# Performance work log

Measured on AMD Instinct MI355X. Metric: run time of the kernel, lower is better.

## Reference

```python
import jax, jax.numpy as jnp
import numpy as np

B, S, D, H, L, DFF, NI, AD = 8, 512, 512, 8, 4, 2048, 20000, 128
DK = D // H


def _make_pe(max_len, d):
    pos = np.arange(max_len, dtype=np.float32)[:, None]
    div = np.exp(np.arange(0, d, 2, dtype=np.float32) * (-np.log(10000.0) / d))
    pe = np.zeros((max_len, d), dtype=np.float32)
    pe[:, 0::2] = np.sin(pos * div)
    pe[:, 1::2] = np.cos(pos * div)
    return jnp.asarray(pe)


def setup_inputs() -> dict:
    key = jax.random.key(0)
    ks = iter(jax.random.split(key, 64))
    def nrm(shape):
        return jax.random.normal(next(ks), shape, jnp.float32) * 0.02
    inp = {
        'item_ids': jax.random.randint(next(ks), (B, S), 0, NI),
        'audio_features': jax.random.normal(next(ks), (B, S, AD), jnp.float32),
        'is_organic': jax.random.bernoulli(next(ks), 0.5, (B, S)).astype(jnp.float32),
        'padding_mask': jnp.ones((B, 1, 1, S), jnp.float32),
        'emb_table': nrm((NI + 1, D)),
        'pe': _make_pe(S, D),
        'Wa1': nrm((AD, D)), 'ba1': jnp.zeros((D,)),
        'Wa2': nrm((D, D)), 'ba2': jnp.zeros((D,)),
        'Wf': nrm((2 * D, D)), 'bf': jnp.zeros((D,)),
        'Wq': nrm((L, D, D)), 'bq': jnp.zeros((L, D)),
        'Wk': nrm((L, D, D)), 'bk': jnp.zeros((L, D)),
        'Wv': nrm((L, D, D)), 'bv': jnp.zeros((L, D)),
        'Wo': nrm((L, D, D)), 'bo': jnp.zeros((L, D)),
        'worg': nrm((L, H)), 'borg': jnp.zeros((L, H)),
        'ln1s': jnp.ones((L, D)), 'ln1b': jnp.zeros((L, D)),
        'ln2s': jnp.ones((L, D)), 'ln2b': jnp.zeros((L, D)),
        'Wff1': nrm((L, D, DFF)), 'bff1': jnp.zeros((L, DFF)),
        'Wff2': nrm((L, DFF, D)), 'bff2': jnp.zeros((L, D)),
        'lnOs': jnp.ones((D,)), 'lnOb': jnp.zeros((D,)),
        'Wg': nrm((D + 1, D)), 'bg': jnp.zeros((D,)),
        'Wout': nrm((D, NI)), 'bout': jnp.zeros((NI,)),
    }
    return inp


def _ln(x, s, b, eps=1e-5):
    m = jnp.mean(x, -1, keepdims=True)
    v = jnp.mean((x - m) ** 2, -1, keepdims=True)
    return (x - m) * jax.lax.rsqrt(v + eps) * s + b


def reference(item_ids, audio_features, is_organic, padding_mask, emb_table, pe,
              Wa1, ba1, Wa2, ba2, Wf, bf, Wq, bq, Wk, bk, Wv, bv, Wo, bo,
              worg, borg, ln1s, ln1b, ln2s, ln2b, Wff1, bff1, Wff2, bff2,
              lnOs, lnOb, Wg, bg, Wout, bout):
    b_, s_ = item_ids.shape
    scale = 1.0 / np.sqrt(DK).astype(np.float32)
    tbl = emb_table.at[0].set(0.0)  # padding_idx=0
    item_emb = tbl[item_ids]                                    # (B,S,D)
    audio_emb = jax.nn.relu(audio_features @ Wa1 + ba1) @ Wa2 + ba2
    x = jax.nn.relu(jnp.concatenate([item_emb, audio_emb], -1) @ Wf + bf)
    x = x + pe[:s_]
    for l in range(L):
        q = (x @ Wq[l] + bq[l]).reshape(b_, s_, H, DK).transpose(0, 2, 1, 3)
        k = (x @ Wk[l] + bk[l]).reshape(b_, s_, H, DK).transpose(0, 2, 1, 3)
        v = (x @ Wv[l] + bv[l]).reshape(b_, s_, H, DK).transpose(0, 2, 1, 3)
        scores = jnp.einsum('bhqd,bhkd->bhqk', q, k) * scale    # (B,H,S,S)
        org = is_organic[:, :, None] * worg[l] + borg[l]        # (B,S,H)
        scores = scores + org.transpose(0, 2, 1)[..., None]     # per-query bias
        scores = jnp.where(padding_mask == 0, -1e9, scores)
        attn = jax.nn.softmax(scores, -1)
        ctx = jnp.einsum('bhqk,bhkd->bhqd', attn, v)
        ctx = ctx.transpose(0, 2, 1, 3).reshape(b_, s_, D)
        x = _ln(x + ctx @ Wo[l] + bo[l], ln1s[l], ln1b[l])
        ff = jax.nn.relu(x @ Wff1[l] + bff1[l]) @ Wff2[l] + bff2[l]
        x = _ln(x + ff, ln2s[l], ln2b[l])
    x = _ln(x, lnOs, lnOb)
    gate = jax.nn.sigmoid(jnp.concatenate([x, is_organic[..., None]], -1) @ Wg + bg)
    logits = (x * gate) @ Wout + bout                           # (B,S,NI)
    return logits
```

## Files before the change

### kernel.cpp

```cpp
#include <hip/hip_runtime.h>
#include <hip/hip_bf16.h>

typedef float f32x4 __attribute__((ext_vector_type(4)));
typedef __bf16 bf16x8 __attribute__((ext_vector_type(8)));

#define DEV __device__ __forceinline__

constexpr int B_ = 8, S_ = 512, D_ = 512, H_ = 8, L_ = 4, DFF_ = 2048, NI_ = 20000, AD_ = 128, DK_ = 64;
constexpr int N_ = B_ * S_;
constexpr int NOUT_PAD = 20096;

DEV void gload_lds16(const void* g, void* l) {
  __builtin_amdgcn_global_load_lds((const __attribute__((address_space(1))) unsigned int*)g,
                                   (__attribute__((address_space(3))) unsigned int*)l, 16, 0, 0);
}

DEV int xcd_swizzle(int bid, int nwg) {
  int q = nwg >> 3, r = nwg & 7;
  int x = bid & 7, idx = bid >> 3;
  int base = (x < r) ? x * (q + 1) : r * (q + 1) + (x - r) * q;
  return base + idx;
}

template<int BM, int BN, int EPI, int ACT, int NT>
__global__ __launch_bounds__(256)
void gemm2(const __hip_bfloat16* __restrict__ A, int lda,
           const __hip_bfloat16* __restrict__ Bm, int ldb,
           void* __restrict__ Cv, int ldc,
           const float* __restrict__ bias,
           const void* __restrict__ p1, const void* __restrict__ p2,
           const void* __restrict__ p3,
           int K, int Ncols)
{
  constexpr int BK = 64;
  constexpr int MI = BM / 32, NJ = BN / 32;
  constexpr int LA = BM * BK / 2048, LB = BN * BK / 2048;
  __shared__ __align__(16) unsigned short smA[2][BM * BK];
  __shared__ __align__(16) unsigned short smB[2][BN * BK];

  const int nwg = gridDim.x * gridDim.y;
  const int bid = blockIdx.y * gridDim.x + blockIdx.x;
  const int wgid = xcd_swizzle(bid, nwg);
  const int m0 = (wgid % gridDim.x) * BM, n0 = (wgid / gridDim.x) * BN;

  const int tid = threadIdx.x, wv = tid >> 6, lane = tid & 63;
  const int l15 = lane & 15, l4 = lane >> 4;
  const int wm = (wv >> 1) * (BM / 2), wn = (wv & 1) * (BN / 2);

  auto stage = [&](int buf, int k0) {
#pragma unroll
    for (int it = 0; it < LA; ++it) {
      int idx = it * 256 + tid, row = idx >> 3, c = idx & 7;
      int sc = c ^ (row & 7);
      gload_lds16((const void*)(A + (size_t)(m0 + row) * lda + k0 + sc * 8),
                  (void*)&smA[buf][(size_t)(it * 256 + wv * 64) * 8]);
    }
#pragma unroll
    for (int it = 0; it < LB; ++it) {
      int idx = it * 256 + tid, row = idx >> 3, c = idx & 7;
      int sc = c ^ (row & 7);
      gload_lds16((const void*)(Bm + (size_t)(n0 + row) * ldb + k0 + sc * 8),
                  (void*)&smB[buf][(size_t)(it * 256 + wv * 64) * 8]);
    }
  };

  f32x4 acc[MI][NJ];
#pragma unroll
  for (int i = 0; i < MI; ++i)
#pragma unroll
    for (int j = 0; j < NJ; ++j) acc[i][j] = f32x4{0.f, 0.f, 0.f, 0.f};

  const int nk = K / BK;
  stage(0, 0);
  __syncthreads();

  int cur = 0;
  for (int t = 0; t < nk; ++t) {
    if (t + 1 < nk) stage(cur ^ 1, (t + 1) * BK);

    bf16x8 af[MI][2], bfr[NJ][2];
#pragma unroll
    for (int i = 0; i < MI; ++i)
#pragma unroll
      for (int kk = 0; kk < 2; ++kk) {
        int row = wm + i * 16 + l15;
        int ch = (kk * 4 + l4) ^ (row & 7);
        af[i][kk] = *reinterpret_cast<const bf16x8*>(&smA[cur][row * BK + ch * 8]);
      }
#pragma unroll
    for (int j = 0; j < NJ; ++j)
#pragma unroll
      for (int kk = 0; kk < 2; ++kk) {
        int row = wn + j * 16 + l15;
        int ch = (kk * 4 + l4) ^ (row & 7);
        bfr[j][kk] = *reinterpret_cast<const bf16x8*>(&smB[cur][row * BK + ch * 8]);
      }
    __builtin_amdgcn_s_setprio(1);
#pragma unroll
    for (int kk = 0; kk < 2; ++kk)
#pragma unroll
      for (int i = 0; i < MI; ++i)
#pragma unroll
        for (int j = 0; j < NJ; ++j)
          acc[i][j] = __builtin_amdgcn_mfma_f32_16x16x32_bf16(af[i][kk], bfr[j][kk], acc[i][j], 0, 0, 0);
    __builtin_amdgcn_s_setprio(0);
    __syncthreads();
    cur ^= 1;
  }

#pragma unroll
  for (int i = 0; i < MI; ++i) {
#pragma unroll
    for (int j = 0; j < NJ; ++j) {
#pragma unroll
      for (int r = 0; r < 4; ++r) {
        int row = m0 + wm + i * 16 + l4 * 4 + r;
        int col = n0 + wn + j * 16 + l15;
        if (col < Ncols) {
          float v = acc[i][j][r];
          if (bias) v += bias[col];
          if (ACT == 1) v = v > 0.f ? v : 0.f;
          if constexpr (EPI == 0) {
            float* dst = &((float*)Cv)[(size_t)row * ldc + col];
            if constexpr (NT) __builtin_nontemporal_store(v, dst);
            else *dst = v;
          } else if constexpr (EPI == 1) {
            ((__hip_bfloat16*)Cv)[(size_t)row * ldc + col] = __float2bfloat16(v);
          } else if constexpr (EPI == 2) {
            v += ((const float*)p2)[(size_t)(row & 511) * 512 + col];
            ((float*)Cv)[(size_t)row * ldc + col] = v;
            ((__hip_bfloat16*)p1)[(size_t)row * ldc + col] = __float2bfloat16(v);
          } else if constexpr (EPI == 3) {
            if (col < 1024) {
              ((__hip_bfloat16*)Cv)[(size_t)(col >> 9) * N_ * 512 + (size_t)row * 512 + (col & 511)] =
                  __float2bfloat16(v);
            } else {
              int hd = col - 1024, b = row >> 9, s = row & 511;
              ((__hip_bfloat16*)p1)[((size_t)(b * 8 + (hd >> 6)) * 64 + (hd & 63)) * 512 + s] =
                  __float2bfloat16(v);
            }
          } else if constexpr (EPI == 4) {
            float zz = v + ((const float*)p2)[row] * ((const float*)p3)[col];
            float sg = 1.f / (1.f + __expf(-zz));
            float xn = ((const float*)p1)[(size_t)row * 512 + col];
            ((__hip_bfloat16*)Cv)[(size_t)row * 512 + col] = __float2bfloat16(xn * sg);
          }
        }
      }
    }
  }
}

__global__ __launch_bounds__(256)
void k_flash(const __hip_bfloat16* __restrict__ q, const __hip_bfloat16* __restrict__ k,
             const __hip_bfloat16* __restrict__ vt, const float* __restrict__ mask,
             __hip_bfloat16* __restrict__ ctx)
{
  __shared__ __align__(16) unsigned short Ql[64 * 64];
  __shared__ __align__(16) unsigned short Kl[2][64 * 64];
  __shared__ __align__(16) unsigned short Vl[2][64 * 64];
  __shared__ __align__(16) unsigned short Pl[4][16 * 64];

  const int qt = blockIdx.x, bh = blockIdx.y;
  const int b = bh >> 3, h = bh & 7;
  const int tid = threadIdx.x, wv = tid >> 6, lane = tid & 63;
  const int l15 = lane & 15, l4 = lane >> 4;
  const int q0 = qt * 64;

  const __hip_bfloat16* Qg = q + ((size_t)(b * 512 + q0) * 512) + h * 64;
  const __hip_bfloat16* Kg = k + ((size_t)(b * 512) * 512) + h * 64;
  const __hip_bfloat16* Vg = vt + ((size_t)bh * 64) * 512;
  const float* mk = mask + b * 512;

  auto stageQ = [&]() {
#pragma unroll
    for (int it = 0; it < 2; ++it) {
      int idx = it * 256 + wv * 64 + lane;
      int row = idx >> 3, c = idx & 7;
      gload_lds16((const void*)(Qg + (size_t)row * 512 + (c ^ (row & 7)) * 8),
                  (void*)&Ql[(it * 256 + wv * 64) * 8]);
    }
  };
  auto stageKV = [&](int buf, int kv0) {
#pragma unroll
    for (int it = 0; it < 2; ++it) {
      int idx = it * 256 + wv * 64 + lane;
      int row = idx >> 3, c = idx & 7;
      gload_lds16((const void*)(Kg + (size_t)(kv0 + row) * 512 + (c ^ (row & 7)) * 8),
                  (void*)&Kl[buf][(it * 256 + wv * 64) * 8]);
    }
#pragma unroll
    for (int it = 0; it < 2; ++it) {
      int idx = it * 256 + wv * 64 + lane;
      int row = idx >> 3, c = idx & 7;
      gload_lds16((const void*)(Vg + (size_t)row * 512 + kv0 + (c ^ (row & 7)) * 8),
                  (void*)&Vl[buf][(it * 256 + wv * 64) * 8]);
    }
  };

  stageQ();
  stageKV(0, 0);
  __syncthreads();

  bf16x8 aq[2];
#pragma unroll
  for (int kk = 0; kk < 2; ++kk) {
    int row = wv * 16 + l15;
    aq[kk] = *reinterpret_cast<const bf16x8*>(
        &Ql[row * 64 + (((kk * 4 + l4) ^ (row & 7)) * 8)]);
  }

  f32x4 accO[4];
  float mrun[4], lrun[4];
#pragma unroll
  for (int j = 0; j < 4; ++j) accO[j] = f32x4{0.f, 0.f, 0.f, 0.f};
#pragma unroll
  for (int r = 0; r < 4; ++r) { mrun[r] = -3e38f; lrun[r] = 0.f; }

  int cur = 0;
  for (int t = 0; t < 8; ++t) {
    if (t + 1 < 8) stageKV(cur ^ 1, (t + 1) * 64);
    const int kv0 = t * 64;

    f32x4 s[4];
#pragma unroll
    for (int j = 0; j < 4; ++j) s[j] = f32x4{0.f, 0.f, 0.f, 0.f};
#pragma unroll
    for (int kk = 0; kk < 2; ++kk) {
#pragma unroll
      for (int j = 0; j < 4; ++j) {
        int row = j * 16 + l15;
        bf16x8 bk = *reinterpret_cast<const bf16x8*>(
            &Kl[cur][row * 64 + (((kk * 4 + l4) ^ (row & 7)) * 8)]);
        s[j] = __builtin_amdgcn_mfma_f32_16x16x32_bf16(aq[kk], bk, s[j], 0, 0, 0);
      }
    }

#pragma unroll
    for (int j = 0; j < 4; ++j) {
      float mval = mk[kv0 + j * 16 + l15];
#pragma unroll
      for (int r = 0; r < 4; ++r)
        s[j][r] = (mval == 0.f) ? -1e30f : s[j][r];
    }

    float alpha[4];
#pragma unroll
    for (int r = 0; r < 4; ++r) {
      float v = fmaxf(fmaxf(s[0][r], s[1][r]), fmaxf(s[2][r], s[3][r]));
      v = fmaxf(v, __shfl_xor(v, 1));
      v = fmaxf(v, __shfl_xor(v, 2));
      v = fmaxf(v, __shfl_xor(v, 4));
      v = fmaxf(v, __shfl_xor(v, 8));
      float mn = fmaxf(mrun[r], v);
      alpha[r] = __expf(mrun[r] - mn);
      mrun[r] = mn;
    }
    float rs[4] = {0.f, 0.f, 0.f, 0.f};
#pragma unroll
    for (int j = 0; j < 4; ++j)
#pragma unroll
      for (int r = 0; r < 4; ++r) {
        float p = __expf(s[j][r] - mrun[r]);
        s[j][r] = p;
        rs[r] += p;
      }
#pragma unroll
    for (int r = 0; r < 4; ++r) {
      float v = rs[r];
      v += __shfl_xor(v, 1); v += __shfl_xor(v, 2);
      v += __shfl_xor(v, 4); v += __shfl_xor(v, 8);
      lrun[r] = lrun[r] * alpha[r] + v;
#pragma unroll
      for (int j = 0; j < 4; ++j) accO[j][r] *= alpha[r];
    }

#pragma unroll
    for (int j = 0; j < 4; ++j)
#pragma unroll
      for (int r = 0; r < 4; ++r) {
        int qrow = l4 * 4 + r, key = j * 16 + l15;
        __hip_bfloat16 hb = __float2bfloat16(s[j][r]);
        Pl[wv][qrow * 64 + (((key >> 3) ^ (qrow & 7)) * 8) + (key & 7)] =
            *reinterpret_cast<unsigned short*>(&hb);
      }

#pragma unroll
    for (int kc = 0; kc < 2; ++kc) {
      bf16x8 ap = *reinterpret_cast<const bf16x8*>(
          &Pl[wv][l15 * 64 + (((kc * 4 + l4) ^ (l15 & 7)) * 8)]);
#pragma unroll
      for (int j = 0; j < 4; ++j) {
        int row = j * 16 + l15;
        bf16x8 bv2 = *reinterpret_cast<const bf16x8*>(
            &Vl[cur][row * 64 + (((kc * 4 + l4) ^ (row & 7)) * 8)]);
        accO[j] = __builtin_amdgcn_mfma_f32_16x16x32_bf16(ap, bv2, accO[j], 0, 0, 0);
      }
    }
    __syncthreads();
    cur ^= 1;
  }

#pragma unroll
  for (int r = 0; r < 4; ++r) {
    float inv = lrun[r] > 0.f ? 1.f / lrun[r] : 0.f;
#pragma unroll
    for (int j = 0; j < 4; ++j) {
      int row = q0 + wv * 16 + l4 * 4 + r;
      int col = h * 64 + j * 16 + l15;
      ctx[(size_t)(b * 512 + row) * 512 + col] = __float2bfloat16(accO[j][r] * inv);
    }
  }
}

__global__ void k_transpose(const float* __restrict__ in, __hip_bfloat16* __restrict__ out,
                            int K, int N, long inBatch, long outBatch, float scale)
{
  __shared__ float tile[32][33];
  int z = blockIdx.z;
  const float* ip = in + (long)z * inBatch;
  __hip_bfloat16* op = out + (long)z * outBatch;
  int n0 = blockIdx.x * 32, k0 = blockIdx.y * 32;
  int tx = threadIdx.x, ty = threadIdx.y;
#pragma unroll
  for (int r = 0; r < 4; ++r) {
    int k = k0 + ty + r * 8, n = n0 + tx;
    if (k < K && n < N) tile[ty + r * 8][tx] = ip[(size_t)k * N + n];
  }
  __syncthreads();
#pragma unroll
  for (int r = 0; r < 4; ++r) {
    int n = n0 + ty + r * 8, k = k0 + tx;
    if (n < N && k < K) op[(size_t)n * K + k] = __float2bfloat16(tile[tx][ty + r * 8] * scale);
  }
}

__global__ void k_cvt(const float* __restrict__ in, __hip_bfloat16* __restrict__ out) {
  int i = blockIdx.x * 256 + threadIdx.x;
  out[i] = __float2bfloat16(in[i]);
}

__global__ void k_packbias(const float* __restrict__ bq, const float* __restrict__ bk,
                           const float* __restrict__ bv, float* __restrict__ out) {
  int i = blockIdx.x * 256 + threadIdx.x;
  int d = i & 511, t = (i >> 9) % 3, l = i / (3 * 512);
  const float* src = (t == 0) ? bq : (t == 1) ? bk : bv;
  out[i] = src[l * 512 + d] * (t == 0 ? 0.125f : 1.f);
}

__global__ void k_gather(const int* __restrict__ ids, const float* __restrict__ tbl,
                         __hip_bfloat16* __restrict__ cat) {
  int n = blockIdx.x, t = threadIdx.x;
  int id = ids[n];
  const float* src = tbl + (size_t)id * 512;
  size_t dst = (size_t)n * 1024;
  float a0 = (id == 0) ? 0.f : src[t];
  float a1 = (id == 0) ? 0.f : src[t + 256];
  cat[dst + t] = __float2bfloat16(a0);
  cat[dst + t + 256] = __float2bfloat16(a1);
}

__global__ void k_ln(const float* __restrict__ x, const float* __restrict__ y,
                     const float* __restrict__ gam, const float* __restrict__ bet,
                     float* __restrict__ xout, __hip_bfloat16* __restrict__ xb) {
  int row = blockIdx.x, t = threadIdx.x;
  size_t base = (size_t)row * 512;
  float v0 = x[base + t], v1 = x[base + t + 256];
  if (y) { v0 += y[base + t]; v1 += y[base + t + 256]; }
  __shared__ float sm[4];
  float s = v0 + v1;
  for (int o = 32; o; o >>= 1) s += __shfl_xor(s, o);
  if ((t & 63) == 0) sm[t >> 6] = s;
  __syncthreads();
  float mean = (sm[0] + sm[1] + sm[2] + sm[3]) * (1.f / 512.f);
  __syncthreads();
  float d0 = v0 - mean, d1 = v1 - mean;
  float qq = d0 * d0 + d1 * d1;
  for (int o = 32; o; o >>= 1) qq += __shfl_xor(qq, o);
  if ((t & 63) == 0) sm[t >> 6] = qq;
  __syncthreads();
  float var = (sm[0] + sm[1] + sm[2] + sm[3]) * (1.f / 512.f);
  float rs = rsqrtf(var + 1e-5f);
  float o0 = d0 * rs * gam[t] + bet[t];
  float o1 = d1 * rs * gam[t + 256] + bet[t + 256];
  xout[base + t] = o0;
  xout[base + t + 256] = o1;
  xb[base + t] = __float2bfloat16(o0);
  xb[base + t + 256] = __float2bfloat16(o1);
}

extern "C" void kernel_launch(void* const* d_in, const int* in_sizes, int n_in,
                              void* d_out, int out_size, void* d_ws, size_t ws_size,
                              hipStream_t stream) {
  typedef __hip_bfloat16 bf;
  const int*   item_ids = (const int*)  d_in[0];
  const float* audio    = (const float*)d_in[1];
  const float* organic  = (const float*)d_in[2];
  const float* mask     = (const float*)d_in[3];
  const float* emb      = (const float*)d_in[4];
  const float* pe       = (const float*)d_in[5];
  const float* Wa1 = (const float*)d_in[6],  *ba1 = (const float*)d_in[7];
  const float* Wa2 = (const float*)d_in[8],  *ba2 = (const float*)d_in[9];
  const float* Wf  = (const float*)d_in[10], *bfb = (const float*)d_in[11];
  const float* Wq  = (const float*)d_in[12], *bq  = (const float*)d_in[13];
  const float* Wk  = (const float*)d_in[14], *bk  = (const float*)d_in[15];
  const float* Wv  = (const float*)d_in[16], *bv  = (const float*)d_in[17];
  const float* Wo  = (const float*)d_in[18], *bo  = (const float*)d_in[19];
  const float* ln1s = (const float*)d_in[22], *ln1b = (const float*)d_in[23];
  const float* ln2s = (const float*)d_in[24], *ln2b = (const float*)d_in[25];
  const float* Wff1 = (const float*)d_in[26], *bff1 = (const float*)d_in[27];
  const float* Wff2 = (const float*)d_in[28], *bff2 = (const float*)d_in[29];
  const float* lnOs = (const float*)d_in[30], *lnOb = (const float*)d_in[31];
  const float* Wg   = (const float*)d_in[32], *bg   = (const float*)d_in[33];
  const float* Wout = (const float*)d_in[34], *bout = (const float*)d_in[35];
  float* out = (float*)d_out;

  char* ws = (char*)d_ws;
  size_t off = 0;
  auto alloc = [&](size_t bytes) -> char* {
    char* p = ws + off;
    off = (off + bytes + 255) & ~(size_t)255;
    return p;
  };
  bf* Wa1T = (bf*)alloc((size_t)512 * 128 * 2);
  bf* Wa2T = (bf*)alloc((size_t)512 * 512 * 2);
  bf* WfT  = (bf*)alloc((size_t)512 * 1024 * 2);
  bf* WqkvT = (bf*)alloc((size_t)L_ * 3 * D_ * D_ * 2);
  bf* WoT  = (bf*)alloc((size_t)L_ * D_ * D_ * 2);
  bf* Wff1T = (bf*)alloc((size_t)L_ * DFF_ * D_ * 2);
  bf* Wff2T = (bf*)alloc((size_t)L_ * D_ * DFF_ * 2);
  bf* WgT   = (bf*)alloc((size_t)512 * 512 * 2);
  bf* WoutT = (bf*)alloc((size_t)NOUT_PAD * 512 * 2);
  float* bqkv = (float*)alloc((size_t)L_ * 3 * 512 * 4);
  bf* ab    = (bf*)alloc((size_t)N_ * AD_ * 2);
  bf* cat   = (bf*)alloc((size_t)N_ * 1024 * 2);
  bf* ah    = (bf*)alloc((size_t)N_ * 512 * 2);
  float* xf = (float*)alloc((size_t)N_ * 512 * 4);
  bf* xb    = (bf*)alloc((size_t)N_ * 512 * 2);
  bf* qkv   = (bf*)alloc((size_t)3 * N_ * 512 * 2);
  bf* vt    = (bf*)alloc((size_t)B_ * H_ * DK_ * S_ * 2);
  bf* ctxb  = (bf*)alloc((size_t)N_ * 512 * 2);
  float* ybuf = (float*)alloc((size_t)N_ * 512 * 4);
  bf* ff1b  = (bf*)alloc((size_t)N_ * DFF_ * 2);
  bf* xg    = (bf*)alloc((size_t)N_ * 512 * 2);
  if (off > ws_size) return;

  bf* qb = qkv;
  bf* kb = qkv + (size_t)N_ * 512;

  dim3 tb(32, 8);
  k_transpose<<<dim3(16, 4, 1),  tb, 0, stream>>>(Wa1, Wa1T, 128, 512, 0, 0, 1.f);
  k_transpose<<<dim3(16, 16, 1), tb, 0, stream>>>(Wa2, Wa2T, 512, 512, 0, 0, 1.f);
  k_transpose<<<dim3(16, 32, 1), tb, 0, stream>>>(Wf, WfT, 1024, 512, 0, 0, 1.f);
  k_transpose<<<dim3(16, 16, L_), tb, 0, stream>>>(Wq, WqkvT, 512, 512,
      (long)D_ * D_, (long)3 * D_ * D_, 0.125f);
  k_transpose<<<dim3(16, 16, L_), tb, 0, stream>>>(Wk, WqkvT + (size_t)D_ * D_, 512, 512,
      (long)D_ * D_, (long)3 * D_ * D_, 1.f);
  k_transpose<<<dim3(16, 16, L_), tb, 0, stream>>>(Wv, WqkvT + (size_t)2 * D_ * D_, 512, 512,
      (long)D_ * D_, (long)3 * D_ * D_, 1.f);
  k_transpose<<<dim3(16, 16, L_), tb, 0, stream>>>(Wo, WoT, 512, 512, (long)D_ * D_, (long)D_ * D_, 1.f);
  k_transpose<<<dim3(64, 16, L_), tb, 0, stream>>>(Wff1, Wff1T, 512, 2048, (long)D_ * DFF_, (long)D_ * DFF_, 1.f);
  k_transpose<<<dim3(16, 64, L_), tb, 0, stream>>>(Wff2, Wff2T, 2048, 512, (long)DFF_ * D_, (long)DFF_ * D_, 1.f);
  k_transpose<<<dim3(16, 16, 1), tb, 0, stream>>>(Wg, WgT, 512, 512, 0, 0, 1.f);
  k_transpose<<<dim3(625, 16, 1), tb, 0, stream>>>(Wout, WoutT, 512, 20000, 0, 0, 1.f);
  k_packbias<<<(L_ * 3 * 512) / 256, 256, 0, stream>>>(bq, bk, bv, bqkv);

  k_cvt<<<(N_ * AD_) / 256, 256, 0, stream>>>(audio, ab);
  k_gather<<<N_, 256, 0, stream>>>(item_ids, emb, cat);
  gemm2<128, 64, 1, 1, 0><<<dim3(32, 8), 256, 0, stream>>>(ab, 128, Wa1T, 128,
      (void*)ah, 512, ba1, nullptr, nullptr, nullptr, 128, 512);
  gemm2<128, 64, 1, 0, 0><<<dim3(32, 8), 256, 0, stream>>>(ah, 512, Wa2T, 512,
      (void*)(cat + 512), 1024, ba2, nullptr, nullptr, nullptr, 512, 512);
  gemm2<128, 64, 2, 1, 0><<<dim3(32, 8), 256, 0, stream>>>(cat, 1024, WfT, 1024,
      (void*)xf, 512, bfb, (void*)xb, (const void*)pe, nullptr, 1024, 512);

  for (int l = 0; l < L_; ++l) {
    gemm2<128, 64, 3, 0, 0><<<dim3(32, 24), 256, 0, stream>>>(xb, 512,
        WqkvT + (size_t)l * 3 * D_ * D_, 512, (void*)qkv, 512,
        bqkv + (size_t)l * 3 * 512, (void*)vt, nullptr, nullptr, 512, 1536);
    k_flash<<<dim3(8, B_ * H_), 256, 0, stream>>>(qb, kb, vt, mask, ctxb);
    gemm2<128, 64, 0, 0, 0><<<dim3(32, 8), 256, 0, stream>>>(ctxb, 512,
        WoT + (size_t)l * D_ * D_, 512, (void*)ybuf, 512, bo + l * D_,
        nullptr, nullptr, nullptr, 512, 512);
    k_ln<<<N_, 256, 0, stream>>>(xf, ybuf, ln1s + l * D_, ln1b + l * D_, xf, xb);
    gemm2<128, 128, 1, 1, 0><<<dim3(32, 16), 256, 0, stream>>>(xb, 512,
        Wff1T + (size_t)l * DFF_ * D_, 512, (void*)ff1b, 2048, bff1 + l * DFF_,
        nullptr, nullptr, nullptr, 512, 2048);
    gemm2<128, 64, 0, 0, 0><<<dim3(32, 8), 256, 0, stream>>>(ff1b, 2048,
        Wff2T + (size_t)l * D_ * DFF_, 2048, (void*)ybuf, 512, bff2 + l * D_,
        nullptr, nullptr, nullptr, 2048, 512);
    k_ln<<<N_, 256, 0, stream>>>(xf, ybuf, ln2s + l * D_, ln2b + l * D_, xf, xb);
  }

  k_ln<<<N_, 256, 0, stream>>>(xf, nullptr, lnOs, lnOb, xf, xb);
  gemm2<128, 64, 4, 0, 0><<<dim3(32, 8), 256, 0, stream>>>(xb, 512, WgT, 512,
      (void*)xg, 512, bg, (const void*)xf, (const void*)organic,
      (const void*)(Wg + (size_t)512 * 512), 512, 512);
  gemm2<128, 128, 0, 0, 1><<<dim3(32, 157), 256, 0, stream>>>(xg, 512, WoutT, 512,
      (void*)out, 20000, bout, nullptr, nullptr, nullptr, 512, 20000);
}
```

Measured before the change: 861.1 us.

## Add 256x128 tile GEMM for output projection and fuse audio cast into gather

Adds a dedicated 512-thread GEMM kernel with 256x128 tiles, BK=32 double-buffered LDS staging with XOR swizzle, non-temporal weight loads and stores, and MFMA priority hints, and uses it for the large 20000-column logits projection. It also merges the audio fp32-to-bf16 conversion into the embedding gather kernel, which removes one launch. The larger tile reuses data better on the dominant GEMM but cuts the grid to about 2.5k blocks and raises register pressure; the smaller BK means more syncs per K step.

Result: slower. 906.3 us (+5.3%).

```diff
diff --git a/kernel.cpp b/kernel.cpp
--- a/kernel.cpp
+++ b/kernel.cpp
@@ -13,6 +13,10 @@
 DEV void gload_lds16(const void* g, void* l) {
   __builtin_amdgcn_global_load_lds((const __attribute__((address_space(1))) unsigned int*)g,
                                    (__attribute__((address_space(3))) unsigned int*)l, 16, 0, 0);
+}
+DEV void gload_lds16_nt(const void* g, void* l) {
+  __builtin_amdgcn_global_load_lds((const __attribute__((address_space(1))) unsigned int*)g,
+                                   (__attribute__((address_space(3))) unsigned int*)l, 16, 0, 2);
 }
 
 DEV int xcd_swizzle(int bid, int nwg) {
@@ -20,6 +24,98 @@
   int x = bid & 7, idx = bid >> 3;
   int base = (x < r) ? x * (q + 1) : r * (q + 1) + (x - r) * q;
   return base + idx;
+}
+
+template<int NTB>
+__global__ __launch_bounds__(512)
+void gemm_big(const __hip_bfloat16* __restrict__ A, int lda,
+              const __hip_bfloat16* __restrict__ Bm, int ldb,
+              float* __restrict__ C, int ldc,
+              const float* __restrict__ bias, int K, int Ncols)
+{
+  __shared__ __align__(16) unsigned short smA[2][256 * 32];
+  __shared__ __align__(16) unsigned short smB[2][128 * 32];
+
+  const int nwg = gridDim.x * gridDim.y;
+  const int bid = blockIdx.y * gridDim.x + blockIdx.x;
+  const int wgid = xcd_swizzle(bid, nwg);
+  const int m0 = (wgid % gridDim.x) * 256, n0 = (wgid / gridDim.x) * 128;
+
+  const int tid = threadIdx.x, wv = tid >> 6, lane = tid & 63;
+  const int l15 = lane & 15, l4 = lane >> 4;
+  const int wm = (wv >> 1) * 64, wn = (wv & 1) * 64;
+
+  auto stage = [&](int buf, int k0) {
+#pragma unroll
+    for (int it = 0; it < 2; ++it) {
+      int idx = it * 512 + tid, row = idx >> 2, c = idx & 3;
+      int sc = c ^ ((row >> 1) & 3);
+      gload_lds16((const void*)(A + (size_t)(m0 + row) * lda + k0 + sc * 8),
+                  (void*)&smA[buf][(size_t)(it * 512 + wv * 64) * 8]);
+    }
+    {
+      int row = tid >> 2, c = tid & 3;
+      int sc = c ^ ((row >> 1) & 3);
+      const void* src = (const void*)(Bm + (size_t)(n0 + row) * ldb + k0 + sc * 8);
+      void* dst = (void*)&smB[buf][(size_t)(wv * 64) * 8];
+      if constexpr (NTB) gload_lds16_nt(src, dst);
+      else gload_lds16(src, dst);
+    }
+  };
+
+  f32x4 acc[4][4];
+#pragma unroll
+  for (int i = 0; i < 4; ++i)
+#pragma unroll
+    for (int j = 0; j < 4; ++j) acc[i][j] = f32x4{0.f, 0.f, 0.f, 0.f};
+
+  const int nk = K / 32;
+  stage(0, 0);
+  __syncthreads();
+
+  int cur = 0;
+  for (int t = 0; t < nk; ++t) {
+    if (t + 1 < nk) stage(cur ^ 1, (t + 1) * 32);
+
+    bf16x8 af[4], bfr[4];
+#pragma unroll
+    for (int i = 0; i < 4; ++i) {
+      int row = wm + i * 16 + l15;
+      int ch = l4 ^ ((row >> 1) & 3);
+      af[i] = *reinterpret_cast<const bf16x8*>(&smA[cur][row * 32 + ch * 8]);
+    }
+#pragma unroll
+    for (int j = 0; j < 4; ++j) {
+      int row = wn + j * 16 + l15;
+      int ch = l4 ^ ((row >> 1) & 3);
+      bfr[j] = *reinterpret_cast<const bf16x8*>(&smB[cur][row * 32 + ch * 8]);
+    }
+    __builtin_amdgcn_s_setprio(1);
+#pragma unroll
+    for (int i = 0; i < 4; ++i)
+#pragma unroll
+      for (int j = 0; j < 4; ++j)
+        acc[i][j] = __builtin_amdgcn_mfma_f32_16x16x32_bf16(af[i], bfr[j], acc[i][j], 0, 0, 0);
+    __builtin_amdgcn_s_setprio(0);
+    __syncthreads();
+    cur ^= 1;
+  }
+
+#pragma unroll
+  for (int i = 0; i < 4; ++i) {
+#pragma unroll
+    for (int j = 0; j < 4; ++j) {
+#pragma unroll
+      for (int r = 0; r < 4; ++r) {
+        int row = m0 + wm + i * 16 + l4 * 4 + r;
+        int col = n0 + wn + j * 16 + l15;
+        if (col < Ncols) {
+          float v = acc[i][j][r] + bias[col];
+          __builtin_nontemporal_store(v, &C[(size_t)row * ldc + col]);
+        }
+      }
+    }
+  }
 }
 
 template<int BM, int BN, int EPI, int ACT, int NT>
@@ -335,11 +431,6 @@
   }
 }
 
-__global__ void k_cvt(const float* __restrict__ in, __hip_bfloat16* __restrict__ out) {
-  int i = blockIdx.x * 256 + threadIdx.x;
-  out[i] = __float2bfloat16(in[i]);
-}
-
 __global__ void k_packbias(const float* __restrict__ bq, const float* __restrict__ bk,
                            const float* __restrict__ bv, float* __restrict__ out) {
   int i = blockIdx.x * 256 + threadIdx.x;
@@ -348,8 +439,9 @@
   out[i] = src[l * 512 + d] * (t == 0 ? 0.125f : 1.f);
 }
 
-__global__ void k_gather(const int* __restrict__ ids, const float* __restrict__ tbl,
-                         __hip_bfloat16* __restrict__ cat) {
+__global__ void k_front(const int* __restrict__ ids, const float* __restrict__ tbl,
+                        const float* __restrict__ audio,
+                        __hip_bfloat16* __restrict__ cat, __hip_bfloat16* __restrict__ ab) {
   int n = blockIdx.x, t = threadIdx.x;
   int id = ids[n];
   const float* src = tbl + (size_t)id * 512;
@@ -358,6 +450,7 @@
   float a1 = (id == 0) ? 0.f : src[t + 256];
   cat[dst + t] = __float2bfloat16(a0);
   cat[dst + t + 256] = __float2bfloat16(a1);
+  if (t < 128) ab[(size_t)n * 128 + t] = __float2bfloat16(audio[(size_t)n * 128 + t]);
 }
 
 __global__ void k_ln(const float* __restrict__ x, const float* __restrict__ y,
@@ -465,8 +558,7 @@
   k_transpose<<<dim3(625, 16, 1), tb, 0, stream>>>(Wout, WoutT, 512, 20000, 0, 0, 1.f);
   k_packbias<<<(L_ * 3 * 512) / 256, 256, 0, stream>>>(bq, bk, bv, bqkv);
 
-  k_cvt<<<(N_ * AD_) / 256, 256, 0, stream>>>(audio, ab);
-  k_gather<<<N_, 256, 0, stream>>>(item_ids, emb, cat);
+  k_front<<<N_, 256, 0, stream>>>(item_ids, emb, audio, cat, ab);
   gemm2<128, 64, 1, 1, 0><<<dim3(32, 8), 256, 0, stream>>>(ab, 128, Wa1T, 128,
       (void*)ah, 512, ba1, nullptr, nullptr, nullptr, 128, 512);
   gemm2<128, 64, 1, 0, 0><<<dim3(32, 8), 256, 0, stream>>>(ah, 512, Wa2T, 512,
@@ -496,6 +588,6 @@
   gemm2<128, 64, 4, 0, 0><<<dim3(32, 8), 256, 0, stream>>>(xb, 512, WgT, 512,
       (void*)xg, 512, bg, (const void*)xf, (const void*)organic,
       (const void*)(Wg + (size_t)512 * 512), 512, 512);
-  gemm2<128, 128, 0, 0, 1><<<dim3(32, 157), 256, 0, stream>>>(xg, 512, WoutT, 512,
-      (void*)out, 20000, bout, nullptr, nullptr, nullptr, 512, 20000);
-}
+  gemm_big<1><<<dim3(16, 157), 512, 0, stream>>>(xg, 512, WoutT, 512,
+      out, 20000, bout, 512, 20000);
+}
```
